# Kernel optimization log

Measured on AMD Instinct MI355X. Metric: run time of the kernel, lower is better.

## Reference

```python
import jax, jax.numpy as jnp
import numpy as np

EPS = 1e-8
LN_EPS = 1e-5  # torch LayerNorm default


def _l2norm(x):
    # L2-norm along last dim, keepdim, clamped at 1e-8 (matches _l2_norm)
    return jnp.maximum(jnp.sqrt(jnp.sum(x * x, axis=-1, keepdims=True)), 1e-8)


def _ln(x, g, b, n_axes):
    # LayerNorm over the last n_axes dims with elementwise affine
    axes = tuple(range(x.ndim - n_axes, x.ndim))
    mu = jnp.mean(x, axis=axes, keepdims=True)
    var = jnp.var(x, axis=axes, keepdims=True)
    return (x - mu) / jnp.sqrt(var + LN_EPS) * g + b


def _get_zs(x, Wk, bk, Wv, bv, zg, zb, sg, sb):
    z = jax.nn.elu(x @ Wk + bk)                     # (B,L,D)
    v = x @ Wv + bv                                  # (B,L,D)
    s = jnp.einsum('blp,blq->blpq', z, v)            # (B,L,D,D)
    z = jnp.cumsum(z, axis=1)
    s = jnp.cumsum(s, axis=1)
    return _ln(z + EPS, zg, zb, 1), _ln(s + EPS, sg, sb, 2)


def setup_inputs() -> dict:
    key = jax.random.key(0)
    ks = jax.random.split(key, 16)
    B, L, LP, IN, D, NU = 16, 512, 8, 64, 64, 1024
    w = lambda k, sh: (jax.random.normal(k, sh, dtype=jnp.float32) * 0.05)
    inp = {
        'user_id': jax.random.randint(ks[0], (B,), 0, NU),
        'seqs_emb': jax.random.normal(ks[1], (B, L, IN), dtype=jnp.float32),
        'P': jax.random.normal(ks[2], (B, LP, IN), dtype=jnp.float32),
        'S': jax.random.normal(ks[3], (B, LP, IN), dtype=jnp.float32),
        'Wq': w(ks[4], (IN, D)), 'bq': jnp.zeros((D,), jnp.float32),
        'Wk': w(ks[5], (IN, D)), 'bk': jnp.zeros((D,), jnp.float32),
        'Wv': w(ks[6], (IN, D)), 'bv': jnp.zeros((D,), jnp.float32),
        'z_g': jnp.ones((D,), jnp.float32), 'z_b': jnp.zeros((D,), jnp.float32),
        's_g': jnp.ones((D, D), jnp.float32), 's_b': jnp.zeros((D, D), jnp.float32),
        'nam_g': jnp.ones((D, D), jnp.float32), 'nam_b': jnp.zeros((D, D), jnp.float32),
        'na_g': jnp.ones((D,), jnp.float32), 'na_b': jnp.zeros((D,), jnp.float32),
        'prev_z_buf': w(ks[7], (NU + 1, D)),
        'prev_s_buf': w(ks[8], (NU + 1, D, D)),
    }
    return inp


def reference(user_id, seqs_emb, P, S, Wq, bq, Wk, bk, Wv, bv,
              z_g, z_b, s_g, s_b, nam_g, nam_b, na_g, na_b,
              prev_z_buf, prev_s_buf):
    q = jax.nn.elu(seqs_emb @ Wq + bq)                          # (B,L,D)
    z, s = _get_zs(seqs_emb, Wk, bk, Wv, bv, z_g, z_b, s_g, s_b)
    # prompt P: add last-step cumulative state
    P_z, P_s = _get_zs(P, Wk, bk, Wv, bv, z_g, z_b, s_g, s_b)
    z = z + P_z[:, -1:, :]
    s = s + P_s[:, -1:, :, :]
    # CSN path (use_csn=True): q normalized with detached norm
    norm_q = q / jax.lax.stop_gradient(_l2norm(q))
    nam = s / _l2norm(z)[..., None]                             # (B,L,D,D)
    na = jnp.einsum('bld,bldp->blp', norm_q, _ln(nam + EPS, nam_g, nam_b, 2))
    # history path (use_history=True) with prompt S
    S_z, S_s = _get_zs(S, Wk, bk, Wv, bv, z_g, z_b, s_g, s_b)
    prev_z = prev_z_buf[user_id] + S_z[:, -1, :]                # (B,D)
    prev_s = prev_s_buf[user_id] + S_s[:, -1, :, :]             # (B,D,D)
    prev_nam = prev_s / (_l2norm(prev_z)[..., None] + EPS)
    prev_na = jnp.einsum('blp,bpq->blq', norm_q, _ln(prev_nam + EPS, nam_g, nam_b, 2))
    na = na + prev_na  # dropout is identity in eval mode
    na = _ln(na, na_g, na_b, 1)
    # unbiased std over all elements (torch.std default)
    std = jnp.std(q / jnp.maximum(z, 1e-6), ddof=1)
    return na, std
```

## Files before the change

### kernel.cpp

```cpp
#include <hip/hip_runtime.h>
#include <math.h>

#define B_ 16
#define L_ 512
#define IN_ 64
#define D_ 64
#define LP_ 8

#define LN_EPS 1e-5f
#define EPSF 1e-8f

__device__ __forceinline__ float wredf(float v){
    #pragma unroll
    for (int o = 32; o; o >>= 1) v += __shfl_xor(v, o, 64);
    return v;
}
__device__ __forceinline__ double wredd(double v){
    #pragma unroll
    for (int o = 32; o; o >>= 1) v += __shfl_xor(v, o, 64);
    return v;
}

__global__ __launch_bounds__(256) void k0_qzv(
    const float* __restrict__ X,
    const float* __restrict__ Wq, const float* __restrict__ bq,
    const float* __restrict__ Wk, const float* __restrict__ bk,
    const float* __restrict__ Wv, const float* __restrict__ bv,
    float* __restrict__ Q, float* __restrict__ Z, float* __restrict__ V,
    double* __restrict__ qstats)
{
    __shared__ float sW[3][IN_*D_];
    __shared__ float sx[4][IN_];
    int t = threadIdx.x;
    if (blockIdx.x == 0 && t < 2) qstats[t] = 0.0;
    for (int i = t; i < IN_*D_; i += 256){ sW[0][i]=Wq[i]; sW[1][i]=Wk[i]; sW[2][i]=Wv[i]; }
    int p = t & 63, lr = t >> 6;
    float bqv = bq[p], bkv = bk[p], bvv = bv[p];
    for (int it = 0; it < 4; ++it){
        int r0 = blockIdx.x*16 + it*4;
        __syncthreads();
        for (int i = t; i < 4*IN_; i += 256)
            sx[i>>6][i&63] = X[(size_t)(r0 + (i>>6))*IN_ + (i&63)];
        __syncthreads();
        size_t row = r0 + lr;
        float aq = bqv, ak = bkv, av = bvv;
        #pragma unroll
        for (int i = 0; i < IN_; i++){
            float x = sx[lr][i];
            aq = fmaf(x, sW[0][i*D_+p], aq);
            ak = fmaf(x, sW[1][i*D_+p], ak);
            av = fmaf(x, sW[2][i*D_+p], av);
        }
        Q[row*D_+p] = aq > 0.f ? aq : (expf(aq)-1.f);
        Z[row*D_+p] = ak > 0.f ? ak : (expf(ak)-1.f);
        V[row*D_+p] = av;
    }
}

__global__ __launch_bounds__(256) void k1_prompt(
    const float* __restrict__ Pm, const float* __restrict__ Sm,
    const float* __restrict__ Wk, const float* __restrict__ bk,
    const float* __restrict__ Wv, const float* __restrict__ bv,
    const float* __restrict__ z_g, const float* __restrict__ z_b,
    const float* __restrict__ s_g, const float* __restrict__ s_b,
    const float* __restrict__ nam_g, const float* __restrict__ nam_b,
    const int* __restrict__ user_id,
    const float* __restrict__ prev_z_buf, const float* __restrict__ prev_s_buf,
    float* __restrict__ Pz, float* __restrict__ Ps, float* __restrict__ prevLN)
{
    __shared__ float sz[LP_][D_], sv[LP_][D_];
    __shared__ double lds[4][2];
    __shared__ float sca[1];
    int blk = blockIdx.x; int b = blk & (B_-1); int path = blk >> 4;
    int t = threadIdx.x, g = t >> 6, p = t & 63;
    const float* Xs = (path ? Sm : Pm) + (size_t)b*LP_*IN_;
    for (int idx = t; idx < 2*LP_*D_; idx += 256){
        int which = idx >> 9;
        int j = (idx >> 6) & 7;
        int d = idx & 63;
        const float* W = which ? Wv : Wk;
        float acc = which ? bv[d] : bk[d];
        const float* xr = Xs + j*IN_;
        #pragma unroll
        for (int i = 0; i < IN_; i++) acc = fmaf(xr[i], W[i*D_+d], acc);
        if (!which) acc = acc > 0.f ? acc : (expf(acc)-1.f);
        if (which) sv[j][d] = acc; else sz[j][d] = acc;
    }
    __syncthreads();
    if (t < 64){
        float zc = 0.f;
        #pragma unroll
        for (int j = 0; j < LP_; j++) zc += sz[j][t];
        double s1 = wredd((double)zc), s2 = wredd((double)zc*(double)zc);
        float mz = (float)(s1*(1.0/64));
        float vz = (float)(s2*(1.0/64) - (s1*(1.0/64))*(s1*(1.0/64)));
        float zf = fmaf((zc-mz)*rsqrtf(vz+LN_EPS), z_g[t], z_b[t]);
        if (path == 0){ Pz[b*D_+t] = zf; }
        else {
            int uid = user_id[b];
            float pz = prev_z_buf[(size_t)uid*D_+t] + zf;
            float rr = wredf(pz*pz);
            if (t == 0) sca[0] = fmaxf(sqrtf(rr), 1e-8f) + EPSF;
        }
    }
    float sc[16];
    #pragma unroll
    for (int i = 0; i < 16; i++){
        int d = g*16 + i; float a = 0.f;
        #pragma unroll
        for (int j = 0; j < LP_; j++) a = fmaf(sz[j][d], sv[j][p], a);
        sc[i] = a;
    }
    double m0 = 0, m1 = 0;
    #pragma unroll
    for (int i = 0; i < 16; i++){ double a = sc[i]; m0 += a; m1 += a*a; }
    m0 = wredd(m0); m1 = wredd(m1);
    __syncthreads();
    if (p == 0){ lds[g][0] = m0; lds[g][1] = m1; }
    __syncthreads();
    m0 = lds[0][0]+lds[1][0]+lds[2][0]+lds[3][0];
    m1 = lds[0][1]+lds[1][1]+lds[2][1]+lds[3][1];
    double mean1 = m0*(1.0/4096.0);
    double var1 = m1*(1.0/4096.0) - mean1*mean1;
    float inv1 = rsqrtf((float)var1 + LN_EPS);
    float mean1f = (float)mean1;
    float sl[16];
    #pragma unroll
    for (int i = 0; i < 16; i++){
        int e = (g*16+i)*D_ + p;
        sl[i] = fmaf((sc[i]-mean1f)*inv1, s_g[e], s_b[e]);
    }
    if (path == 0){
        #pragma unroll
        for (int i = 0; i < 16; i++) Ps[(size_t)b*4096 + (g*16+i)*D_ + p] = sl[i];
        return;
    }
    int uid = user_id[b];
    float denom = sca[0];
    float pn[16]; double n0 = 0, n1 = 0;
    #pragma unroll
    for (int i = 0; i < 16; i++){
        int e = (g*16+i)*D_ + p;
        float ps = prev_s_buf[(size_t)uid*4096 + e] + sl[i];
        float v = ps / denom;
        pn[i] = v; n0 += v; n1 += (double)v*(double)v;
    }
    n0 = wredd(n0); n1 = wredd(n1);
    __syncthreads();
    if (p == 0){ lds[g][0] = n0; lds[g][1] = n1; }
    __syncthreads();
    n0 = lds[0][0]+lds[1][0]+lds[2][0]+lds[3][0];
    n1 = lds[0][1]+lds[1][1]+lds[2][1]+lds[3][1];
    double meanp = n0*(1.0/4096.0);
    double varp = n1*(1.0/4096.0) - meanp*meanp;
    float invp = rsqrtf((float)varp + LN_EPS);
    float meanpf = (float)meanp;
    #pragma unroll
    for (int i = 0; i < 16; i++){
        int e = (g*16+i)*D_ + p;
        prevLN[(size_t)b*4096 + e] = fmaf((pn[i]-meanpf)*invp, nam_g[e], nam_b[e]);
    }
}

__global__ __launch_bounds__(256) void k2_chunks(
    const float* __restrict__ Z, const float* __restrict__ V,
    float* __restrict__ spart, float* __restrict__ zpart, int C_, int LC_)
{
    int wg = blockIdx.x; int b = wg / C_, c = wg - b*C_;
    int t = threadIdx.x, g = t >> 6, p = t & 63;
    __shared__ float lz[64], lv[64];
    float acc[16];
    #pragma unroll
    for (int i = 0; i < 16; i++) acc[i] = 0.f;
    float zacc = 0.f;
    for (int l = 0; l < LC_; l++){
        size_t row = (size_t)b*L_ + c*LC_ + l;
        __syncthreads();
        if (t < 64) lz[t] = Z[row*64 + t];
        else if (t < 128) lv[t-64] = V[row*64 + (t-64)];
        __syncthreads();
        float v = lv[p];
        #pragma unroll
        for (int i = 0; i < 16; i++) acc[i] = fmaf(lz[g*16+i], v, acc[i]);
        if (t < 64) zacc += lz[t];
    }
    size_t base = ((size_t)wg) << 12;
    #pragma unroll
    for (int i = 0; i < 16; i++) spart[base + (g*16+i)*64 + p] = acc[i];
    if (t < 64) zpart[(size_t)wg*64 + t] = zacc;
}

__global__ __launch_bounds__(256) void k3_prefix(
    float* __restrict__ spart, float* __restrict__ zpart, int C_)
{
    int id = blockIdx.x*256 + threadIdx.x;
    const int NS = B_*4096;
    if (id < NS){
        int b = id >> 12;
        int e = id & 4095;
        float run = 0.f;
        for (int c = 0; c < C_; ++c){
            float* ptr = spart + (((size_t)(b*C_+c)) << 12) + e;
            float tv = *ptr; *ptr = run; run += tv;
        }
    } else if (id < NS + B_*64){
        int k = id - NS;
        int b = k >> 6, d = k & 63;
        float run = 0.f;
        for (int c = 0; c < C_; ++c){
            float* ptr = zpart + (size_t)(b*C_+c)*64 + d;
            float tv = *ptr; *ptr = run; run += tv;
        }
    }
}

__global__ __launch_bounds__(256) void k4_main(
    const float* __restrict__ Q, const float* __restrict__ Z, const float* __restrict__ V,
    const float* __restrict__ spart, const float* __restrict__ zpart,
    const float* __restrict__ Pz, const float* __restrict__ Ps,
    const float* __restrict__ prevLN,
    const float* __restrict__ z_g, const float* __restrict__ z_b,
    const float* __restrict__ s_g, const float* __restrict__ s_b,
    const float* __restrict__ nam_g, const float* __restrict__ nam_b,
    const float* __restrict__ na_g, const float* __restrict__ na_b,
    float* __restrict__ out, double* qstats, int C_, int LC_)
{
    int wg = blockIdx.x; int b = wg / C_, c = wg - b*C_;
    int t = threadIdx.x, g = t >> 6, p = t & 63;
    __shared__ float lz[64], lv[64], lq[64], lnq[64], lPz[64], lna[4][64];
    __shared__ float lr[1];
    __shared__ double lmd[4][6];
    float A[16], Gv[16], Bv[16], NGv[16], NBv[16];
    size_t sbase = ((size_t)wg) << 12;
    size_t bbase = ((size_t)b) << 12;
    #pragma unroll
    for (int i = 0; i < 16; i++){
        int e = (g*16+i)*64 + p;
        A[i]   = spart[sbase + e];
        Gv[i]  = s_g[e];
        Bv[i]  = s_b[e] + Ps[bbase + e];
        NGv[i] = nam_g[e];
        NBv[i] = nam_b[e] + prevLN[bbase + e];
    }
    double cs[5] = {0,0,0,0,0};
    #pragma unroll
    for (int i = 0; i < 16; i++){
        double gd = Gv[i], bd = Bv[i];
        cs[0] += gd; cs[1] += gd*gd; cs[2] += bd; cs[3] += bd*bd; cs[4] += gd*bd;
    }
    #pragma unroll
    for (int k = 0; k < 5; k++) cs[k] = wredd(cs[k]);
    if (p == 0){
        #pragma unroll
        for (int k = 0; k < 5; k++) lmd[g][k] = cs[k];
    }
    __syncthreads();
    #pragma unroll
    for (int k = 0; k < 5; k++) cs[k] = lmd[0][k]+lmd[1][k]+lmd[2][k]+lmd[3][k];
    double Cg = cs[0], Cg2 = cs[1], Cb = cs[2], Cb2 = cs[3], Cgb = cs[4];

    float zc = 0.f, zgr = 0.f, zbr = 0.f, nagr = 0.f, nabr = 0.f;
    if (g == 0){
        zc  = zpart[(size_t)wg*64 + p];
        lPz[p] = Pz[b*64 + p];
        zgr = z_g[p]; zbr = z_b[p];
        nagr = na_g[p]; nabr = na_b[p];
    }
    double qsum = 0.0, qsq = 0.0;
    const double INV = 1.0/4096.0;
    for (int ll = 0; ll < LC_; ++ll){
        int l = c*LC_ + ll;
        size_t row = (size_t)b*L_ + l;
        __syncthreads();
        if (t < 64) lz[t] = Z[row*64 + t];
        else if (t < 128) lv[t-64] = V[row*64 + (t-64)];
        else if (t < 192) lq[t-128] = Q[row*64 + (t-128)];
        __syncthreads();
        if (g == 0){
            float zl = lz[p]; zc += zl;
            double s1 = wredd((double)zc), s2 = wredd((double)zc*(double)zc);
            double mzd = s1*(1.0/64);
            float mz = (float)mzd;
            float vz = (float)(s2*(1.0/64) - mzd*mzd);
            float zf = fmaf((zc-mz)*rsqrtf(vz+LN_EPS), zgr, zbr) + lPz[p];
            float rr = wredf(zf*zf);
            if (p == 0) lr[0] = fmaxf(sqrtf(rr), 1e-8f);
            float qv = lq[p];
            float qn = qv / fmaxf(zf, 1e-6f);
            qsum += (double)qn; qsq += (double)qn*(double)qn;
            float qq = wredf(qv*qv);
            lnq[p] = qv / fmaxf(sqrtf(qq), 1e-8f);
        }
        double m[6] = {0,0,0,0,0,0};
        float vp = lv[p];
        #pragma unroll
        for (int i = 0; i < 16; i++){
            A[i] = fmaf(lz[g*16+i], vp, A[i]);
            double a = (double)A[i];
            m[0] += a; m[1] += a*a;
            double tt = a*(double)Gv[i];
            m[2] += tt; m[5] += tt*tt; m[3] += tt*(double)Gv[i]; m[4] += tt*(double)Bv[i];
        }
        #pragma unroll
        for (int k = 0; k < 6; k++) m[k] = wredd(m[k]);
        if (p == 0){
            #pragma unroll
            for (int k = 0; k < 6; k++) lmd[g][k] = m[k];
        }
        __syncthreads();
        #pragma unroll
        for (int k = 0; k < 6; k++) m[k] = lmd[0][k]+lmd[1][k]+lmd[2][k]+lmd[3][k];
        double meanA = m[0]*INV;
        double varA  = m[1]*INV - meanA*meanA;
        float inv1 = rsqrtf((float)varA + LN_EPS);
        double inv1d = (double)inv1;
        double sum_sf = inv1d*(m[2] - meanA*Cg) + Cb;
        double ssq_sf = inv1d*inv1d*(m[5] - 2.0*meanA*m[3] + meanA*meanA*Cg2)
                      + 2.0*inv1d*(m[4] - meanA*Cgb) + Cb2;
        float r = lr[0];
        float invr = 1.f/r;
        double mean_sf = sum_sf*INV;
        double var_sf  = ssq_sf*INV - mean_sf*mean_sf;
        float mean_nam = (float)mean_sf * invr;
        float var_nam  = (float)var_sf * invr * invr;
        float inv2 = rsqrtf(var_nam + LN_EPS);
        float meanAf = (float)meanA;
        float nal = 0.f;
        #pragma unroll
        for (int i = 0; i < 16; i++){
            float sf = fmaf((A[i]-meanAf)*inv1, Gv[i], Bv[i]);
            float nm = sf*invr;
            float elem = fmaf((nm-mean_nam)*inv2, NGv[i], NBv[i]);
            nal = fmaf(lnq[g*16+i], elem, nal);
        }
        lna[g][p] = nal;
        __syncthreads();
        if (g == 0){
            float nt = lna[0][p]+lna[1][p]+lna[2][p]+lna[3][p];
            float s1 = wredf(nt), s2 = wredf(nt*nt);
            float mu = s1*(1.f/64.f);
            float va = s2*(1.f/64.f) - mu*mu;
            out[row*64 + p] = fmaf((nt-mu)*rsqrtf(va+LN_EPS), nagr, nabr);
        }
    }
    if (g == 0){
        double s = wredd(qsum), s2 = wredd(qsq);
        if (p == 0){
            atomicAdd(&qstats[0], s);
            atomicAdd(&qstats[1], s2);
        }
    }
}

__global__ void k5_std(const double* __restrict__ qstats, float* __restrict__ out, int idx){
    if (threadIdx.x == 0 && blockIdx.x == 0){
        double s = qstats[0], sq = qstats[1];
        const double N = (double)(B_*L_*D_);
        double var = (sq - s*s/N) / (N - 1.0);
        out[idx] = (float)sqrt(var > 0.0 ? var : 0.0);
    }
}

extern "C" void kernel_launch(void* const* d_in, const int* in_sizes, int n_in,
                              void* d_out, int out_size, void* d_ws, size_t ws_size,
                              hipStream_t stream)
{
    (void)in_sizes; (void)n_in;
    const int*   user_id    = (const int*)d_in[0];
    const float* seqs       = (const float*)d_in[1];
    const float* Pm         = (const float*)d_in[2];
    const float* Sm         = (const float*)d_in[3];
    const float* Wq         = (const float*)d_in[4];
    const float* bq         = (const float*)d_in[5];
    const float* Wk         = (const float*)d_in[6];
    const float* bk         = (const float*)d_in[7];
    const float* Wv         = (const float*)d_in[8];
    const float* bv         = (const float*)d_in[9];
    const float* z_g        = (const float*)d_in[10];
    const float* z_b        = (const float*)d_in[11];
    const float* s_g        = (const float*)d_in[12];
    const float* s_b        = (const float*)d_in[13];
    const float* nam_g      = (const float*)d_in[14];
    const float* nam_b      = (const float*)d_in[15];
    const float* na_g       = (const float*)d_in[16];
    const float* na_b       = (const float*)d_in[17];
    const float* prev_z_buf = (const float*)d_in[18];
    const float* prev_s_buf = (const float*)d_in[19];
    float* out = (float*)d_out;

    char* w = (char*)d_ws;
    double* qstats = (double*)w;
    float* Q  = (float*)(w + 16);
    float* Zb = Q  + 524288;
    float* Vb = Zb + 524288;
    float* Pz = Vb + 524288;
    float* Ps = Pz + 1024;
    float* prevLN = Ps + 65536;
    float* spart  = prevLN + 65536;
    size_t fixedBytes = 16 + (size_t)(3*524288 + 1024 + 2*65536)*4;
    int C = 64;
    while (C > 1 && fixedBytes + (size_t)16*C*(4096+64)*4 > ws_size) C >>= 1;
    int LC = 512 / C;
    float* zpart = spart + (size_t)16*C*4096;

    k0_qzv<<<512, 256, 0, stream>>>(seqs, Wq, bq, Wk, bk, Wv, bv, Q, Zb, Vb, qstats);
    k1_prompt<<<32, 256, 0, stream>>>(Pm, Sm, Wk, bk, Wv, bv, z_g, z_b, s_g, s_b,
                                      nam_g, nam_b, user_id, prev_z_buf, prev_s_buf,
                                      Pz, Ps, prevLN);
    k2_chunks<<<16*C, 256, 0, stream>>>(Zb, Vb, spart, zpart, C, LC);
    k3_prefix<<<(16*4096 + 16*64 + 255)/256, 256, 0, stream>>>(spart, zpart, C);
    k4_main<<<16*C, 256, 0, stream>>>(Q, Zb, Vb, spart, zpart, Pz, Ps, prevLN,
                                      z_g, z_b, s_g, s_b, nam_g, nam_b, na_g, na_b,
                                      out, qstats, C, LC);
    k5_std<<<1, 64, 0, stream>>>(qstats, out, out_size - 1);
}
```

Measured before the change: 232.1 us.

## Fuse chunk outer-product into projection kernel and pipeline main loop loads

Fuses the per-chunk z⊗v partial sums into the QKV projection kernel so the separate chunk kernel and its re-read of Z/V disappear. The prefix scan now loads all chunks into registers before scanning. The main kernel double-buffers its Q/Z/V rows with direct global-to-LDS loads, drops one barrier per row by deferring the output LayerNorm by one step, spreads work across waves, and switches the LayerNorm statistics from double to float. The float switch risks losing precision in the moment-based variance formulas, which involve cancellation.

```diff
diff --git a/kernel.cpp b/kernel.cpp
--- a/kernel.cpp
+++ b/kernel.cpp
@@ -1,5 +1,6 @@
 #include <hip/hip_runtime.h>
 #include <math.h>
+#include <stdint.h>
 
 #define B_ 16
 #define L_ 512
@@ -21,39 +22,73 @@
     return v;
 }
 
-__global__ __launch_bounds__(256) void k0_qzv(
+__device__ __forceinline__ void gl_lds4(const float* gsrc, float* ldst){
+    __builtin_amdgcn_global_load_lds((const __attribute__((address_space(1))) void*)gsrc,
+                                     (__attribute__((address_space(3))) void*)ldst, 4, 0, 0);
+}
+
+template<int LC, int NCH>
+__global__ __launch_bounds__(256) void k0_fused(
     const float* __restrict__ X,
     const float* __restrict__ Wq, const float* __restrict__ bq,
     const float* __restrict__ Wk, const float* __restrict__ bk,
     const float* __restrict__ Wv, const float* __restrict__ bv,
     float* __restrict__ Q, float* __restrict__ Z, float* __restrict__ V,
+    float* __restrict__ spart, float* __restrict__ zpart,
     double* __restrict__ qstats)
 {
     __shared__ float sW[3][IN_*D_];
     __shared__ float sx[4][IN_];
+    __shared__ float sz[16][D_], sv[16][D_];
     int t = threadIdx.x;
     if (blockIdx.x == 0 && t < 2) qstats[t] = 0.0;
     for (int i = t; i < IN_*D_; i += 256){ sW[0][i]=Wq[i]; sW[1][i]=Wk[i]; sW[2][i]=Wv[i]; }
-    int p = t & 63, lr = t >> 6;
+    int p = t & 63, g = t >> 6;
     float bqv = bq[p], bkv = bk[p], bvv = bv[p];
+    int r0 = blockIdx.x * 16;
     for (int it = 0; it < 4; ++it){
-        int r0 = blockIdx.x*16 + it*4;
-        __syncthreads();
-        for (int i = t; i < 4*IN_; i += 256)
-            sx[i>>6][i&63] = X[(size_t)(r0 + (i>>6))*IN_ + (i&63)];
-        __syncthreads();
-        size_t row = r0 + lr;
+        __syncthreads();
+        sx[g][p] = X[(size_t)(r0 + it*4 + g)*IN_ + p];
+        __syncthreads();
+        int lrow = it*4 + g;
+        size_t row = r0 + lrow;
         float aq = bqv, ak = bkv, av = bvv;
         #pragma unroll
         for (int i = 0; i < IN_; i++){
-            float x = sx[lr][i];
+            float x = sx[g][i];
             aq = fmaf(x, sW[0][i*D_+p], aq);
             ak = fmaf(x, sW[1][i*D_+p], ak);
             av = fmaf(x, sW[2][i*D_+p], av);
         }
-        Q[row*D_+p] = aq > 0.f ? aq : (expf(aq)-1.f);
-        Z[row*D_+p] = ak > 0.f ? ak : (expf(ak)-1.f);
-        V[row*D_+p] = av;
+        aq = aq > 0.f ? aq : (expf(aq)-1.f);
+        ak = ak > 0.f ? ak : (expf(ak)-1.f);
+        Q[row*D_+p] = aq; Z[row*D_+p] = ak; V[row*D_+p] = av;
+        sz[lrow][p] = ak; sv[lrow][p] = av;
+    }
+    __syncthreads();
+    int b = r0 >> 9;
+    int c0 = (r0 & 511) / LC;
+    #pragma unroll
+    for (int ch = 0; ch < NCH; ch++){
+        float acc[16];
+        #pragma unroll
+        for (int i = 0; i < 16; i++) acc[i] = 0.f;
+        #pragma unroll
+        for (int l = 0; l < LC; l++){
+            float vv = sv[ch*LC+l][p];
+            #pragma unroll
+            for (int i = 0; i < 16; i++) acc[i] = fmaf(sz[ch*LC+l][g*16+i], vv, acc[i]);
+        }
+        size_t cg = (size_t)(b*(512/LC) + c0 + ch);
+        size_t base = cg << 12;
+        #pragma unroll
+        for (int i = 0; i < 16; i++) spart[base + (g*16+i)*64 + p] = acc[i];
+        if (g == 0){
+            float za = 0.f;
+            #pragma unroll
+            for (int l = 0; l < LC; l++) za += sz[ch*LC+l][p];
+            zpart[cg*64 + p] = za;
+        }
     }
 }
 
@@ -162,6 +197,72 @@
     }
 }
 
+template<int C>
+__global__ __launch_bounds__(256) void k3_scan(
+    float* __restrict__ spart, float* __restrict__ zpart)
+{
+    int id = blockIdx.x*256 + threadIdx.x;
+    const int NS = B_*4096;
+    if (id < NS){
+        int b = id >> 12, e = id & 4095;
+        float a[C];
+        #pragma unroll
+        for (int c = 0; c < C; c++) a[c] = spart[(((size_t)(b*C+c)) << 12) + e];
+        float run = 0.f;
+        #pragma unroll
+        for (int c = 0; c < C; c++){ float tv = a[c]; a[c] = run; run += tv; }
+        #pragma unroll
+        for (int c = 0; c < C; c++) spart[(((size_t)(b*C+c)) << 12) + e] = a[c];
+    } else if (id < NS + B_*64){
+        int k = id - NS;
+        int b = k >> 6, d = k & 63;
+        float a[C];
+        #pragma unroll
+        for (int c = 0; c < C; c++) a[c] = zpart[(size_t)(b*C+c)*64 + d];
+        float run = 0.f;
+        #pragma unroll
+        for (int c = 0; c < C; c++){ float tv = a[c]; a[c] = run; run += tv; }
+        #pragma unroll
+        for (int c = 0; c < C; c++) zpart[(size_t)(b*C+c)*64 + d] = a[c];
+    }
+}
+
+__global__ __launch_bounds__(256) void k0_qzv(
+    const float* __restrict__ X,
+    const float* __restrict__ Wq, const float* __restrict__ bq,
+    const float* __restrict__ Wk, const float* __restrict__ bk,
+    const float* __restrict__ Wv, const float* __restrict__ bv,
+    float* __restrict__ Q, float* __restrict__ Z, float* __restrict__ V,
+    double* __restrict__ qstats)
+{
+    __shared__ float sW[3][IN_*D_];
+    __shared__ float sx[4][IN_];
+    int t = threadIdx.x;
+    if (blockIdx.x == 0 && t < 2) qstats[t] = 0.0;
+    for (int i = t; i < IN_*D_; i += 256){ sW[0][i]=Wq[i]; sW[1][i]=Wk[i]; sW[2][i]=Wv[i]; }
+    int p = t & 63, lr = t >> 6;
+    float bqv = bq[p], bkv = bk[p], bvv = bv[p];
+    for (int it = 0; it < 4; ++it){
+        int r0 = blockIdx.x*16 + it*4;
+        __syncthreads();
+        for (int i = t; i < 4*IN_; i += 256)
+            sx[i>>6][i&63] = X[(size_t)(r0 + (i>>6))*IN_ + (i&63)];
+        __syncthreads();
+        size_t row = r0 + lr;
+        float aq = bqv, ak = bkv, av = bvv;
+        #pragma unroll
+        for (int i = 0; i < IN_; i++){
+            float x = sx[lr][i];
+            aq = fmaf(x, sW[0][i*D_+p], aq);
+            ak = fmaf(x, sW[1][i*D_+p], ak);
+            av = fmaf(x, sW[2][i*D_+p], av);
+        }
+        Q[row*D_+p] = aq > 0.f ? aq : (expf(aq)-1.f);
+        Z[row*D_+p] = ak > 0.f ? ak : (expf(ak)-1.f);
+        V[row*D_+p] = av;
+    }
+}
+
 __global__ __launch_bounds__(256) void k2_chunks(
     const float* __restrict__ Z, const float* __restrict__ V,
     float* __restrict__ spart, float* __restrict__ zpart, int C_, int LC_)
@@ -190,7 +291,7 @@
     if (t < 64) zpart[(size_t)wg*64 + t] = zacc;
 }
 
-__global__ __launch_bounds__(256) void k3_prefix(
+__global__ __launch_bounds__(256) void k3_serial(
     float* __restrict__ spart, float* __restrict__ zpart, int C_)
 {
     int id = blockIdx.x*256 + threadIdx.x;
@@ -227,12 +328,19 @@
 {
     int wg = blockIdx.x; int b = wg / C_, c = wg - b*C_;
     int t = threadIdx.x, g = t >> 6, p = t & 63;
-    __shared__ float lz[64], lv[64], lq[64], lnq[64], lPz[64], lna[4][64];
-    __shared__ float lr[1];
-    __shared__ double lmd[4][6];
+    __shared__ float lz[2][64], lv[2][64], lqb[2][64], lnq[2][64];
+    __shared__ float lna[2][4][64];
+    __shared__ float lmd[2][4][6];
+    __shared__ float lcs[4][5];
+    __shared__ float lr[2];
+    __shared__ float lPz[64];
     float A[16], Gv[16], Bv[16], NGv[16], NBv[16];
     size_t sbase = ((size_t)wg) << 12;
     size_t bbase = ((size_t)b) << 12;
+    size_t row0 = (size_t)b*L_ + (size_t)c*LC_;
+    if (g == 1) gl_lds4(Q + row0*64 + p, &lqb[0][0]);
+    else if (g == 2) gl_lds4(Z + row0*64 + p, &lz[0][0]);
+    else if (g == 3) gl_lds4(V + row0*64 + p, &lv[0][0]);
     #pragma unroll
     for (int i = 0; i < 16; i++){
         int e = (g*16+i)*64 + p;
@@ -242,106 +350,115 @@
         NGv[i] = nam_g[e];
         NBv[i] = nam_b[e] + prevLN[bbase + e];
     }
-    double cs[5] = {0,0,0,0,0};
+    float cs0=0,cs1=0,cs2=0,cs3=0,cs4=0;
     #pragma unroll
     for (int i = 0; i < 16; i++){
-        double gd = Gv[i], bd = Bv[i];
-        cs[0] += gd; cs[1] += gd*gd; cs[2] += bd; cs[3] += bd*bd; cs[4] += gd*bd;
-    }
-    #pragma unroll
-    for (int k = 0; k < 5; k++) cs[k] = wredd(cs[k]);
-    if (p == 0){
-        #pragma unroll
-        for (int k = 0; k < 5; k++) lmd[g][k] = cs[k];
-    }
-    __syncthreads();
-    #pragma unroll
-    for (int k = 0; k < 5; k++) cs[k] = lmd[0][k]+lmd[1][k]+lmd[2][k]+lmd[3][k];
-    double Cg = cs[0], Cg2 = cs[1], Cb = cs[2], Cb2 = cs[3], Cgb = cs[4];
-
-    float zc = 0.f, zgr = 0.f, zbr = 0.f, nagr = 0.f, nabr = 0.f;
+        float gd = Gv[i], bd = Bv[i];
+        cs0 += gd; cs1 += gd*gd; cs2 += bd; cs3 += bd*bd; cs4 += gd*bd;
+    }
+    cs0=wredf(cs0); cs1=wredf(cs1); cs2=wredf(cs2); cs3=wredf(cs3); cs4=wredf(cs4);
+    if (p == 0){ lcs[g][0]=cs0; lcs[g][1]=cs1; lcs[g][2]=cs2; lcs[g][3]=cs3; lcs[g][4]=cs4; }
+    float zc=0.f, zgr=0.f, zbr=0.f, nagr=0.f, nabr=0.f;
     if (g == 0){
-        zc  = zpart[(size_t)wg*64 + p];
+        zc = zpart[(size_t)wg*64 + p];
         lPz[p] = Pz[b*64 + p];
         zgr = z_g[p]; zbr = z_b[p];
-        nagr = na_g[p]; nabr = na_b[p];
-    }
+    }
+    if (g == 3){ nagr = na_g[p]; nabr = na_b[p]; }
+    __syncthreads();
+    float Cg  = lcs[0][0]+lcs[1][0]+lcs[2][0]+lcs[3][0];
+    float Cg2 = lcs[0][1]+lcs[1][1]+lcs[2][1]+lcs[3][1];
+    float Cb  = lcs[0][2]+lcs[1][2]+lcs[2][2]+lcs[3][2];
+    float Cb2 = lcs[0][3]+lcs[1][3]+lcs[2][3]+lcs[3][3];
+    float Cgb = lcs[0][4]+lcs[1][4]+lcs[2][4]+lcs[3][4];
+
     double qsum = 0.0, qsq = 0.0;
-    const double INV = 1.0/4096.0;
+    const float INV = 1.f/4096.f;
     for (int ll = 0; ll < LC_; ++ll){
-        int l = c*LC_ + ll;
-        size_t row = (size_t)b*L_ + l;
-        __syncthreads();
-        if (t < 64) lz[t] = Z[row*64 + t];
-        else if (t < 128) lv[t-64] = V[row*64 + (t-64)];
-        else if (t < 192) lq[t-128] = Q[row*64 + (t-128)];
-        __syncthreads();
+        int cur = ll & 1, nxt = cur ^ 1, prv = cur ^ 1;
+        size_t row = row0 + ll;
+        if (ll + 1 < LC_){
+            if (g == 1) gl_lds4(Q + (row+1)*64 + p, &lqb[nxt][0]);
+            else if (g == 2) gl_lds4(Z + (row+1)*64 + p, &lz[nxt][0]);
+            else if (g == 3) gl_lds4(V + (row+1)*64 + p, &lv[nxt][0]);
+        }
         if (g == 0){
-            float zl = lz[p]; zc += zl;
-            double s1 = wredd((double)zc), s2 = wredd((double)zc*(double)zc);
-            double mzd = s1*(1.0/64);
-            float mz = (float)mzd;
-            float vz = (float)(s2*(1.0/64) - mzd*mzd);
+            float zl = lz[cur][p]; zc += zl;
+            float s1 = wredf(zc), s2 = wredf(zc*zc);
+            float mz = s1*(1.f/64.f);
+            float vz = s2*(1.f/64.f) - mz*mz;
             float zf = fmaf((zc-mz)*rsqrtf(vz+LN_EPS), zgr, zbr) + lPz[p];
             float rr = wredf(zf*zf);
-            if (p == 0) lr[0] = fmaxf(sqrtf(rr), 1e-8f);
-            float qv = lq[p];
-            float qn = qv / fmaxf(zf, 1e-6f);
+            if (p == 0) lr[cur] = fmaxf(sqrtf(rr), 1e-8f);
+            float qvv = lqb[cur][p];
+            float qn = qvv / fmaxf(zf, 1e-6f);
             qsum += (double)qn; qsq += (double)qn*(double)qn;
-            float qq = wredf(qv*qv);
-            lnq[p] = qv / fmaxf(sqrtf(qq), 1e-8f);
-        }
-        double m[6] = {0,0,0,0,0,0};
-        float vp = lv[p];
+        }
+        if (g == 1){
+            float qvv = lqb[cur][p];
+            float qq = wredf(qvv*qvv);
+            lnq[cur][p] = qvv / fmaxf(sqrtf(qq), 1e-8f);
+        }
+        float m0=0,m1=0,m2=0,m3=0,m4=0,m5=0;
+        float vp = lv[cur][p];
         #pragma unroll
         for (int i = 0; i < 16; i++){
-            A[i] = fmaf(lz[g*16+i], vp, A[i]);
-            double a = (double)A[i];
-            m[0] += a; m[1] += a*a;
-            double tt = a*(double)Gv[i];
-            m[2] += tt; m[5] += tt*tt; m[3] += tt*(double)Gv[i]; m[4] += tt*(double)Bv[i];
-        }
-        #pragma unroll
-        for (int k = 0; k < 6; k++) m[k] = wredd(m[k]);
+            A[i] = fmaf(lz[cur][g*16+i], vp, A[i]);
+            float a = A[i];
+            m0 += a; m1 = fmaf(a, a, m1);
+            float tt = a * Gv[i];
+            m2 += tt; m5 = fmaf(tt, tt, m5); m3 = fmaf(tt, Gv[i], m3); m4 = fmaf(tt, Bv[i], m4);
+        }
+        m0=wredf(m0); m1=wredf(m1); m2=wredf(m2); m3=wredf(m3); m4=wredf(m4); m5=wredf(m5);
         if (p == 0){
-            #pragma unroll
-            for (int k = 0; k < 6; k++) lmd[g][k] = m[k];
-        }
-        __syncthreads();
-        #pragma unroll
-        for (int k = 0; k < 6; k++) m[k] = lmd[0][k]+lmd[1][k]+lmd[2][k]+lmd[3][k];
-        double meanA = m[0]*INV;
-        double varA  = m[1]*INV - meanA*meanA;
-        float inv1 = rsqrtf((float)varA + LN_EPS);
-        double inv1d = (double)inv1;
-        double sum_sf = inv1d*(m[2] - meanA*Cg) + Cb;
-        double ssq_sf = inv1d*inv1d*(m[5] - 2.0*meanA*m[3] + meanA*meanA*Cg2)
-                      + 2.0*inv1d*(m[4] - meanA*Cgb) + Cb2;
-        float r = lr[0];
+            lmd[cur][g][0]=m0; lmd[cur][g][1]=m1; lmd[cur][g][2]=m2;
+            lmd[cur][g][3]=m3; lmd[cur][g][4]=m4; lmd[cur][g][5]=m5;
+        }
+        __syncthreads();
+        float M0 = lmd[cur][0][0]+lmd[cur][1][0]+lmd[cur][2][0]+lmd[cur][3][0];
+        float M1 = lmd[cur][0][1]+lmd[cur][1][1]+lmd[cur][2][1]+lmd[cur][3][1];
+        float M2 = lmd[cur][0][2]+lmd[cur][1][2]+lmd[cur][2][2]+lmd[cur][3][2];
+        float M3 = lmd[cur][0][3]+lmd[cur][1][3]+lmd[cur][2][3]+lmd[cur][3][3];
+        float M4 = lmd[cur][0][4]+lmd[cur][1][4]+lmd[cur][2][4]+lmd[cur][3][4];
+        float M5 = lmd[cur][0][5]+lmd[cur][1][5]+lmd[cur][2][5]+lmd[cur][3][5];
+        float meanA = M0*INV;
+        float varA  = M1*INV - meanA*meanA;
+        float inv1 = rsqrtf(varA + LN_EPS);
+        float sum_sf = inv1*(M2 - meanA*Cg) + Cb;
+        float ssq_sf = inv1*inv1*(M5 - 2.f*meanA*M3 + meanA*meanA*Cg2)
+                     + 2.f*inv1*(M4 - meanA*Cgb) + Cb2;
+        float r = lr[cur];
         float invr = 1.f/r;
-        double mean_sf = sum_sf*INV;
-        double var_sf  = ssq_sf*INV - mean_sf*mean_sf;
-        float mean_nam = (float)mean_sf * invr;
-        float var_nam  = (float)var_sf * invr * invr;
+        float mean_sf = sum_sf*INV;
+        float var_sf  = ssq_sf*INV - mean_sf*mean_sf;
+        float mean_nam = mean_sf * invr;
+        float var_nam  = var_sf * invr * invr;
         float inv2 = rsqrtf(var_nam + LN_EPS);
-        float meanAf = (float)meanA;
         float nal = 0.f;
         #pragma unroll
         for (int i = 0; i < 16; i++){
-            float sf = fmaf((A[i]-meanAf)*inv1, Gv[i], Bv[i]);
+            float sf = fmaf((A[i]-meanA)*inv1, Gv[i], Bv[i]);
             float nm = sf*invr;
             float elem = fmaf((nm-mean_nam)*inv2, NGv[i], NBv[i]);
-            nal = fmaf(lnq[g*16+i], elem, nal);
-        }
-        lna[g][p] = nal;
-        __syncthreads();
-        if (g == 0){
-            float nt = lna[0][p]+lna[1][p]+lna[2][p]+lna[3][p];
+            nal = fmaf(lnq[cur][g*16+i], elem, nal);
+        }
+        lna[cur][g][p] = nal;
+        if (g == 3 && ll > 0){
+            float nt = lna[prv][0][p]+lna[prv][1][p]+lna[prv][2][p]+lna[prv][3][p];
             float s1 = wredf(nt), s2 = wredf(nt*nt);
             float mu = s1*(1.f/64.f);
             float va = s2*(1.f/64.f) - mu*mu;
-            out[row*64 + p] = fmaf((nt-mu)*rsqrtf(va+LN_EPS), nagr, nabr);
-        }
+            out[(row-1)*64 + p] = fmaf((nt-mu)*rsqrtf(va+LN_EPS), nagr, nabr);
+        }
+    }
+    __syncthreads();
+    if (g == 3){
+        int lastc = (LC_-1) & 1;
+        float nt = lna[lastc][0][p]+lna[lastc][1][p]+lna[lastc][2][p]+lna[lastc][3][p];
+        float s1 = wredf(nt), s2 = wredf(nt*nt);
+        float mu = s1*(1.f/64.f);
+        float va = s2*(1.f/64.f) - mu*mu;
+        out[(row0+LC_-1)*64 + p] = fmaf((nt-mu)*rsqrtf(va+LN_EPS), nagr, nabr);
     }
     if (g == 0){
         double s = wredd(qsum), s2 = wredd(qsq);
@@ -403,12 +520,28 @@
     int LC = 512 / C;
     float* zpart = spart + (size_t)16*C*4096;
 
-    k0_qzv<<<512, 256, 0, stream>>>(seqs, Wq, bq, Wk, bk, Wv, bv, Q, Zb, Vb, qstats);
-    k1_prompt<<<32, 256, 0, stream>>>(Pm, Sm, Wk, bk, Wv, bv, z_g, z_b, s_g, s_b,
-                                      nam_g, nam_b, user_id, prev_z_buf, prev_s_buf,
-                                      Pz, Ps, prevLN);
-    k2_chunks<<<16*C, 256, 0, stream>>>(Zb, Vb, spart, zpart, C, LC);
-    k3_prefix<<<(16*4096 + 16*64 + 255)/256, 256, 0, stream>>>(spart, zpart, C);
+    if (C == 64){
+        k0_fused<8,2><<<512, 256, 0, stream>>>(seqs, Wq, bq, Wk, bk, Wv, bv,
+                                               Q, Zb, Vb, spart, zpart, qstats);
+        k1_prompt<<<32, 256, 0, stream>>>(Pm, Sm, Wk, bk, Wv, bv, z_g, z_b, s_g, s_b,
+                                          nam_g, nam_b, user_id, prev_z_buf, prev_s_buf,
+                                          Pz, Ps, prevLN);
+        k3_scan<64><<<(16*4096 + 16*64 + 255)/256, 256, 0, stream>>>(spart, zpart);
+    } else if (C == 32){
+        k0_fused<16,1><<<512, 256, 0, stream>>>(seqs, Wq, bq, Wk, bk, Wv, bv,
+                                                Q, Zb, Vb, spart, zpart, qstats);
+        k1_prompt<<<32, 256, 0, stream>>>(Pm, Sm, Wk, bk, Wv, bv, z_g, z_b, s_g, s_b,
+                                          nam_g, nam_b, user_id, prev_z_buf, prev_s_buf,
+                                          Pz, Ps, prevLN);
+        k3_scan<32><<<(16*4096 + 16*64 + 255)/256, 256, 0, stream>>>(spart, zpart);
+    } else {
+        k0_qzv<<<512, 256, 0, stream>>>(seqs, Wq, bq, Wk, bk, Wv, bv, Q, Zb, Vb, qstats);
+        k1_prompt<<<32, 256, 0, stream>>>(Pm, Sm, Wk, bk, Wv, bv, z_g, z_b, s_g, s_b,
+                                          nam_g, nam_b, user_id, prev_z_buf, prev_s_buf,
+                                          Pz, Ps, prevLN);
+        k2_chunks<<<16*C, 256, 0, stream>>>(Zb, Vb, spart, zpart, C, LC);
+        k3_serial<<<(16*4096 + 16*64 + 255)/256, 256, 0, stream>>>(spart, zpart, C);
+    }
     k4_main<<<16*C, 256, 0, stream>>>(Q, Zb, Vb, spart, zpart, Pz, Ps, prevLN,
                                       z_g, z_b, s_g, s_b, nam_g, nam_b, na_g, na_b,
                                       out, qstats, C, LC);
```

Result: faster. 191.9 us (-17.3%).
